# Optimization experiments

Measured on AMD Instinct MI355X. Metric: run time of the kernel, lower is better.

## Reference

```python
import jax, jax.numpy as jnp
import numpy as np

N_NODES = 50000
N_EDGES = 800000
N_GRAPHS = 1024
H = 128          # hidden_dim
L = 5            # n_conv_layers
NODE_IN = 4
EDGE_IN = 41
N_TARGETS = 3
EPS = 1e-5


def _ln(x, g, b):
    m = jnp.mean(x, axis=-1, keepdims=True)
    v = jnp.var(x, axis=-1, keepdims=True)
    return (x - m) / jnp.sqrt(v + EPS) * g + b


def setup_inputs() -> dict:
    key = jax.random.key(0)
    ks = jax.random.split(key, 24)
    w = lambda k, shp: (jax.random.normal(k, shp, dtype=jnp.float32) * 0.05)
    inp = {
        "atom_fea": jax.random.normal(ks[0], (N_NODES, NODE_IN), dtype=jnp.float32),
        "nbr_fea": jax.random.normal(ks[1], (N_EDGES, EDGE_IN), dtype=jnp.float32),
        "nbr_idx": jax.random.randint(ks[2], (N_EDGES, 2), 0, N_NODES, dtype=jnp.int32),
        "batch_mapping": jnp.sort(jax.random.randint(ks[3], (N_NODES,), 0, N_GRAPHS, dtype=jnp.int32)),
        # node embedding: Linear(4->H) + LayerNorm + SiLU
        "emb_w": w(ks[4], (NODE_IN, H)), "emb_b": jnp.zeros((H,), jnp.float32),
        "emb_ln_g": jnp.ones((H,), jnp.float32), "emb_ln_b": jnp.zeros((H,), jnp.float32),
        # edge embedding: Linear(41->H) + SiLU
        "edge_w": w(ks[5], (EDGE_IN, H)), "edge_b": jnp.zeros((H,), jnp.float32),
        # conv layers: Linear(2H->2H), SiLU, Linear(2H->H), SiLU; stacked over L
        "conv_w1": w(ks[6], (L, 2 * H, 2 * H)), "conv_b1": jnp.zeros((L, 2 * H), jnp.float32),
        "conv_w2": w(ks[7], (L, 2 * H, H)), "conv_b2": jnp.zeros((L, H), jnp.float32),
        "ln_g": jnp.ones((L, H), jnp.float32), "ln_b": jnp.zeros((L, H), jnp.float32),
        # output head
        "out_w1": w(ks[8], (H, H)), "out_b1": jnp.zeros((H,), jnp.float32),
        "out_w2": w(ks[9], (H, H // 2)), "out_b2": jnp.zeros((H // 2,), jnp.float32),
        "out_w3": w(ks[10], (H // 2, N_TARGETS)), "out_b3": jnp.zeros((N_TARGETS,), jnp.float32),
    }
    return inp


def reference(atom_fea, nbr_fea, nbr_idx, batch_mapping,
              emb_w, emb_b, emb_ln_g, emb_ln_b, edge_w, edge_b,
              conv_w1, conv_b1, conv_w2, conv_b2, ln_g, ln_b,
              out_w1, out_b1, out_w2, out_b2, out_w3, out_b3):
    silu = jax.nn.silu
    # embeddings (dropout is eval-mode identity)
    x = silu(_ln(atom_fea @ emb_w + emb_b, emb_ln_g, emb_ln_b))      # [N, H]
    e = silu(nbr_fea @ edge_w + edge_b)                               # [E, H]
    src, dst = nbr_idx[:, 0], nbr_idx[:, 1]
    n = x.shape[0]
    # per-node incoming edge counts (same every layer)
    cnt = jax.ops.segment_sum(jnp.ones_like(dst, dtype=x.dtype), dst, num_segments=n)
    cnt = jnp.clip(cnt, 1.0)[:, None]
    for i in range(L):
        m = jnp.concatenate([x[src], e], axis=1)                      # [E, 2H] gather
        m = silu(m @ conv_w1[i] + conv_b1[i])                         # [E, 2H]
        m = silu(m @ conv_w2[i] + conv_b2[i])                         # [E, H]
        aggr = jax.ops.segment_sum(m, dst, num_segments=n) / cnt      # scatter-mean
        x = _ln(x + aggr, ln_g[i], ln_b[i])                           # residual + LN
    # graph-level mean pooling
    gcnt = jax.ops.segment_sum(jnp.ones((n,), x.dtype), batch_mapping, num_segments=N_GRAPHS)
    gcnt = jnp.clip(gcnt, 1.0)[:, None]
    crystal = jax.ops.segment_sum(x, batch_mapping, num_segments=N_GRAPHS) / gcnt  # [G, H]
    h = silu(crystal @ out_w1 + out_b1)
    h = silu(h @ out_w2 + out_b2)
    return h @ out_w3 + out_b3                                        # [G, n_targets]
```

## Files before the change

kernel.cpp:

```cpp
#include <hip/hip_runtime.h>
#include <hip/hip_bf16.h>
#include <math.h>

#define N_NODES 50000
#define N_EDGES 800000
#define N_GRAPHS 1024
#define HD 128
#define NLAYERS 5
#define EDGE_IN 41
#define NT 3
#define LN_EPS 1e-5f

typedef unsigned int uint;
typedef unsigned short ushort;
typedef __attribute__((ext_vector_type(8))) short short8;
typedef __attribute__((ext_vector_type(4))) float f32x4;

__device__ __forceinline__ float silu_f(float v) {
    return v * __builtin_amdgcn_rcpf(1.0f + __expf(-v));
}

__device__ __forceinline__ ushort f2bf(float f) {
    uint u = __float_as_uint(f);
    u = u + 0x7FFFu + ((u >> 16) & 1u);
    return (ushort)(u >> 16);
}

__device__ __forceinline__ short8 ld16(const ushort* p) {
    union { int4 i; short8 s; } u;
    u.i = *(const int4*)p;
    return u.s;
}

__device__ __forceinline__ f32x4 mfma16(short8 a, short8 b, f32x4 c) {
    return __builtin_amdgcn_mfma_f32_16x16x32_bf16(a, b, c, 0, 0, 0);
}

__device__ __forceinline__ void wave_lds_fence() {
    __asm__ volatile("s_waitcnt lgkmcnt(0)" ::: "memory");
}

__device__ __forceinline__ void cp16(const ushort* g, ushort* l) {
    __builtin_amdgcn_global_load_lds(
        (const __attribute__((address_space(1))) unsigned int*)g,
        (__attribute__((address_space(3))) unsigned int*)l, 16, 0, 0);
}

__device__ __forceinline__ void stage4k(ushort* lds, const ushort* g, int w, int L) {
#pragma unroll
    for (int i = 0; i < 2; ++i) {
        int f = w * 1024 + i * 512;
        cp16(g + f + L * 8, lds + f);
    }
}

__global__ void k_zero(float* __restrict__ p, int n) {
    int i = blockIdx.x * 256 + threadIdx.x;
    if (i < n) p[i] = 0.0f;
}

__global__ void k_swz_w1(const float* __restrict__ w1, ushort* __restrict__ w1s) {
    int i = blockIdx.x * 256 + threadIdx.x;
    int l = i >> 16;
    int r = i & 65535;
    int j = r & 7, L = (r >> 3) & 63, s = (r >> 9) & 7, c = (r >> 12) & 15;
    int k = 32 * s + ((L >> 4) & 3) * 8 + j;
    int n = 16 * c + (L & 15);
    w1s[i] = f2bf(w1[(size_t)l * 65536 + k * 256 + n]);
}
__global__ void k_swz_w2(const float* __restrict__ w2, ushort* __restrict__ w2s) {
    int i = blockIdx.x * 256 + threadIdx.x;
    int l = i >> 15;
    int r = i & 32767;
    int j = r & 7, L = (r >> 3) & 63, t = (r >> 9) & 7, s2 = (r >> 12) & 7;
    int k = 32 * s2 + ((L >> 4) & 3) * 8 + j;
    int n = 16 * t + (L & 15);
    w2s[i] = f2bf(w2[(size_t)l * 32768 + k * 128 + n]);
}

__global__ __launch_bounds__(128) void k_node_embed(
    const float* __restrict__ atom, const float* __restrict__ w,
    const float* __restrict__ b, const float* __restrict__ g,
    const float* __restrict__ bet, float* __restrict__ x, ushort* __restrict__ x_bf)
{
    int node = blockIdx.x;
    int h = threadIdx.x;
    float4 a = *(const float4*)(atom + (size_t)node * 4);
    float acc = b[h] + a.x * w[h] + a.y * w[HD + h] + a.z * w[2 * HD + h] + a.w * w[3 * HD + h];
    __shared__ float s1[2], s2[2];
    float sum = acc, sq = acc * acc;
    for (int off = 32; off > 0; off >>= 1) { sum += __shfl_down(sum, off); sq += __shfl_down(sq, off); }
    int wid = h >> 6, lane = h & 63;
    if (lane == 0) { s1[wid] = sum; s2[wid] = sq; }
    __syncthreads();
    float m = (s1[0] + s1[1]) * (1.0f / 128.0f);
    float v = (s2[0] + s2[1]) * (1.0f / 128.0f) - m * m;
    float y = (acc - m) * rsqrtf(v + LN_EPS) * g[h] + bet[h];
    y = silu_f(y);
    x[(size_t)node * HD + h] = y;
    x_bf[(size_t)node * HD + h] = f2bf(y);
}

#define ETILE 32
__global__ __launch_bounds__(128) void k_edge_embed(
    const float* __restrict__ fea, const float* __restrict__ w,
    const float* __restrict__ b, ushort* __restrict__ e_bf)
{
    __shared__ float sf[ETILE][EDGE_IN + 1];
    int e0 = blockIdx.x * ETILE;
    int tid = threadIdx.x;
    for (int i = tid; i < ETILE * EDGE_IN; i += 128) {
        int m = i / EDGE_IN, k = i % EDGE_IN;
        sf[m][k] = fea[(size_t)(e0 + m) * EDGE_IN + k];
    }
    __syncthreads();
    float bb = b[tid];
    float acc[ETILE];
#pragma unroll
    for (int m = 0; m < ETILE; m++) acc[m] = bb;
    for (int k = 0; k < EDGE_IN; k++) {
        float wk = w[k * HD + tid];
#pragma unroll
        for (int m = 0; m < ETILE; m++) acc[m] += sf[m][k] * wk;
    }
#pragma unroll
    for (int m = 0; m < ETILE; m++)
        e_bf[(size_t)(e0 + m) * HD + tid] = f2bf(silu_f(acc[m]));
}

__global__ void k_count(const int* __restrict__ nbr_idx, float* __restrict__ cnt) {
    int i = blockIdx.x * 256 + threadIdx.x;
    if (i < N_EDGES) atomicAdd(&cnt[nbr_idx[2 * i + 1]], 1.0f);
}
__global__ void k_gcount(const int* __restrict__ bm, float* __restrict__ gcnt) {
    int i = blockIdx.x * 256 + threadIdx.x;
    if (i < N_NODES) atomicAdd(&gcnt[bm[i]], 1.0f);
}

#define M1CP 40
__global__ __launch_bounds__(256, 3) void k_conv_mfma(
    const ushort* __restrict__ x_bf, const ushort* __restrict__ e_bf,
    const int* __restrict__ nbr_idx,
    const ushort* __restrict__ w1s, const float* __restrict__ cb1,
    const ushort* __restrict__ w2s, const float* __restrict__ cb2,
    float* __restrict__ aggr)
{
    __shared__ __align__(16) ushort sW1[2][4096];
    __shared__ __align__(16) ushort sW2[2][4096];
    __shared__ __align__(16) ushort sM1[4][32 * M1CP];
    __shared__ int sDst[128];

    int tid = threadIdx.x;
    int w = tid >> 6;
    int L = tid & 63;
    int m = L & 15;
    int quad = L >> 4;
    int eb = blockIdx.x * 128;
    int ew = eb + w * 32;

    if (tid < 128) sDst[tid] = nbr_idx[2 * (eb + tid) + 1];

    short8 af[2][8];
#pragma unroll
    for (int t = 0; t < 2; ++t) {
        int src = nbr_idx[2 * (ew + t * 16 + m)];
        const ushort* xr = x_bf + (size_t)src * HD + quad * 8;
        const ushort* er = e_bf + (size_t)(ew + t * 16 + m) * HD + quad * 8;
#pragma unroll
        for (int s = 0; s < 4; ++s) af[t][s] = ld16(xr + 32 * s);
#pragma unroll
        for (int s = 0; s < 4; ++s) af[t][4 + s] = ld16(er + 32 * s);
    }

    f32x4 acc2[2][8];
#pragma unroll
    for (int t = 0; t < 2; ++t)
#pragma unroll
        for (int tt = 0; tt < 8; ++tt)
#pragma unroll
            for (int r = 0; r < 4; ++r) acc2[t][tt][r] = 0.0f;

    ushort* sm = sM1[w];

    stage4k(sW1[0], w1s, w, L);
    stage4k(sW2[0], w2s, w, L);

    for (int p = 0; p < 16; ++p) {
        __syncthreads();
        if (p < 15) stage4k(sW1[(p + 1) & 1], w1s + (p + 1) * 4096, w, L);
        if ((p & 1) && (p >> 1) < 7)
            stage4k(sW2[((p >> 1) + 1) & 1], w2s + ((p >> 1) + 1) * 4096, w, L);

        f32x4 p0, p1;
#pragma unroll
        for (int r = 0; r < 4; ++r) { p0[r] = 0.0f; p1[r] = 0.0f; }
        const ushort* wb = sW1[p & 1] + L * 8;
#pragma unroll
        for (int s = 0; s < 8; ++s) {
            short8 wv = ld16(wb + s * 512);
            p0 = mfma16(af[0][s], wv, p0);
            p1 = mfma16(af[1][s], wv, p1);
        }

        float bv = cb1[p * 16 + m];
        int hb = (p & 1) * 16;
#pragma unroll
        for (int r = 0; r < 4; ++r) {
            sm[(quad * 4 + r) * M1CP + hb + m]        = f2bf(silu_f(p0[r] + bv));
            sm[(16 + quad * 4 + r) * M1CP + hb + m]   = f2bf(silu_f(p1[r] + bv));
        }

        if (p & 1) {
            wave_lds_fence();
            short8 a20 = ld16(sm + m * M1CP + quad * 8);
            short8 a21 = ld16(sm + (16 + m) * M1CP + quad * 8);
            const ushort* w2p = sW2[(p >> 1) & 1] + L * 8;
#pragma unroll
            for (int tt = 0; tt < 8; ++tt) {
                short8 bf = ld16(w2p + tt * 512);
                acc2[0][tt] = mfma16(a20, bf, acc2[0][tt]);
                acc2[1][tt] = mfma16(a21, bf, acc2[1][tt]);
            }
            wave_lds_fence();
        }
    }

#pragma unroll
    for (int t = 0; t < 2; ++t) {
#pragma unroll
        for (int tt = 0; tt < 8; ++tt) {
            float bv = cb2[tt * 16 + m];
#pragma unroll
            for (int r = 0; r < 4; ++r) {
                int dst = sDst[w * 32 + t * 16 + quad * 4 + r];
                atomicAdd(aggr + (size_t)dst * HD + tt * 16 + m,
                          silu_f(acc2[t][tt][r] + bv));
            }
        }
    }
}

__global__ __launch_bounds__(128) void k_post(
    float* __restrict__ aggr, const float* __restrict__ cnt,
    const float* __restrict__ g, const float* __restrict__ bet,
    float* __restrict__ x, ushort* __restrict__ x_bf)
{
    int node = blockIdx.x;
    int h = threadIdx.x;
    float inv = __builtin_amdgcn_rcpf(fmaxf(cnt[node], 1.0f));
    float av = aggr[(size_t)node * HD + h];
    aggr[(size_t)node * HD + h] = 0.0f;
    float acc = x[(size_t)node * HD + h] + av * inv;
    __shared__ float s1[2], s2[2];
    float sum = acc, sq = acc * acc;
    for (int off = 32; off > 0; off >>= 1) { sum += __shfl_down(sum, off); sq += __shfl_down(sq, off); }
    int wid = h >> 6, lane = h & 63;
    if (lane == 0) { s1[wid] = sum; s2[wid] = sq; }
    __syncthreads();
    float m = (s1[0] + s1[1]) * (1.0f / 128.0f);
    float v = (s2[0] + s2[1]) * (1.0f / 128.0f) - m * m;
    float y = (acc - m) * rsqrtf(v + LN_EPS) * g[h] + bet[h];
    x[(size_t)node * HD + h] = y;
    x_bf[(size_t)node * HD + h] = f2bf(y);
}

__global__ __launch_bounds__(128) void k_gaggr(
    const float* __restrict__ x, const int* __restrict__ bm,
    float* __restrict__ crystal)
{
    int node = blockIdx.x;
    int h = threadIdx.x;
    atomicAdd(&crystal[(size_t)bm[node] * HD + h], x[(size_t)node * HD + h]);
}

__global__ __launch_bounds__(128) void k_readout(
    const float* __restrict__ crystal, const float* __restrict__ gcnt,
    const float* __restrict__ w1, const float* __restrict__ b1,
    const float* __restrict__ w2, const float* __restrict__ b2,
    const float* __restrict__ w3, const float* __restrict__ b3,
    float* __restrict__ out)
{
    int gph = blockIdx.x;
    int t = threadIdx.x;
    __shared__ float sc[HD], sh1[HD], sh2[64];
    float inv = __builtin_amdgcn_rcpf(fmaxf(gcnt[gph], 1.0f));
    sc[t] = crystal[(size_t)gph * HD + t] * inv;
    __syncthreads();
    float acc = b1[t];
    for (int k = 0; k < HD; k++) acc += sc[k] * w1[k * HD + t];
    sh1[t] = silu_f(acc);
    __syncthreads();
    if (t < 64) {
        float a2 = b2[t];
        for (int k = 0; k < HD; k++) a2 += sh1[k] * w2[k * 64 + t];
        sh2[t] = silu_f(a2);
    }
    __syncthreads();
    if (t < NT) {
        float a3 = b3[t];
        for (int k = 0; k < 64; k++) a3 += sh2[k] * w3[k * NT + t];
        out[(size_t)gph * NT + t] = a3;
    }
}

extern "C" void kernel_launch(void* const* d_in, const int* in_sizes, int n_in,
                              void* d_out, int out_size, void* d_ws, size_t ws_size,
                              hipStream_t stream)
{
    const float* atom_fea = (const float*)d_in[0];
    const float* nbr_fea  = (const float*)d_in[1];
    const int*   nbr_idx  = (const int*)d_in[2];
    const int*   bm       = (const int*)d_in[3];
    const float* emb_w    = (const float*)d_in[4];
    const float* emb_b    = (const float*)d_in[5];
    const float* emb_ln_g = (const float*)d_in[6];
    const float* emb_ln_b = (const float*)d_in[7];
    const float* edge_w   = (const float*)d_in[8];
    const float* edge_b   = (const float*)d_in[9];
    const float* conv_w1  = (const float*)d_in[10];
    const float* conv_b1  = (const float*)d_in[11];
    const float* conv_w2  = (const float*)d_in[12];
    const float* conv_b2  = (const float*)d_in[13];
    const float* ln_g     = (const float*)d_in[14];
    const float* ln_b     = (const float*)d_in[15];
    const float* out_w1   = (const float*)d_in[16];
    const float* out_b1   = (const float*)d_in[17];
    const float* out_w2   = (const float*)d_in[18];
    const float* out_b2   = (const float*)d_in[19];
    const float* out_w3   = (const float*)d_in[20];
    const float* out_b3   = (const float*)d_in[21];
    float* out = (float*)d_out;

    char* base = (char*)d_ws;
    size_t off = 0;
    auto alloc = [&](size_t bytes) -> char* {
        char* p = base + off;
        off = (off + bytes + 255) & ~(size_t)255;
        return p;
    };
    float*  xbuf    = (float*) alloc((size_t)N_NODES * HD * 4);
    float*  aggr    = (float*) alloc((size_t)N_NODES * HD * 4);
    float*  cnt     = (float*) alloc((size_t)N_NODES * 4);
    float*  crystal = (float*) alloc((size_t)N_GRAPHS * HD * 4);
    float*  gcnt    = (float*) alloc((size_t)N_GRAPHS * 4);
    ushort* x_bf    = (ushort*)alloc((size_t)N_NODES * HD * 2);
    ushort* e_bf    = (ushort*)alloc((size_t)N_EDGES * HD * 2);
    ushort* w1s     = (ushort*)alloc((size_t)NLAYERS * 65536 * 2);
    ushort* w2s     = (ushort*)alloc((size_t)NLAYERS * 32768 * 2);

    k_swz_w1<<<(NLAYERS * 65536) / 256, 256, 0, stream>>>(conv_w1, w1s);
    k_swz_w2<<<(NLAYERS * 32768) / 256, 256, 0, stream>>>(conv_w2, w2s);

    k_zero<<<(N_NODES * HD) / 256, 256, 0, stream>>>(aggr, N_NODES * HD);
    int zn = N_NODES + N_GRAPHS * HD + N_GRAPHS + 128;
    k_zero<<<(zn + 255) / 256, 256, 0, stream>>>(cnt, zn);

    k_node_embed<<<N_NODES, 128, 0, stream>>>(atom_fea, emb_w, emb_b, emb_ln_g, emb_ln_b, xbuf, x_bf);
    k_edge_embed<<<N_EDGES / ETILE, 128, 0, stream>>>(nbr_fea, edge_w, edge_b, e_bf);
    k_count<<<N_EDGES / 256, 256, 0, stream>>>(nbr_idx, cnt);
    k_gcount<<<(N_NODES + 255) / 256, 256, 0, stream>>>(bm, gcnt);

    for (int l = 0; l < NLAYERS; ++l) {
        k_conv_mfma<<<N_EDGES / 128, 256, 0, stream>>>(
            x_bf, e_bf, nbr_idx,
            w1s + (size_t)l * 65536, conv_b1 + (size_t)l * 256,
            w2s + (size_t)l * 32768, conv_b2 + (size_t)l * 128,
            aggr);
        k_post<<<N_NODES, 128, 0, stream>>>(aggr, cnt, ln_g + (size_t)l * HD, ln_b + (size_t)l * HD, xbuf, x_bf);
    }

    k_gaggr<<<N_NODES, 128, 0, stream>>>(xbuf, bm, crystal);
    k_readout<<<N_GRAPHS, 128, 0, stream>>>(crystal, gcnt, out_w1, out_b1, out_w2, out_b2, out_w3, out_b3, out);
}
```

Measured before the change: 2.746 ms.

## Sort edges by destination and pre-reduce messages in LDS before atomics

Builds a destination-sorted edge order (histogram, single-block scan, atomic scatter) and writes edge embeddings and src/dst arrays in that order. The conv kernel then stages its output tile in LDS and run-length-sums consecutive edges with the same destination before issuing global atomicAdds. The aim is fewer, more local atomics on aggr. In exchange it adds preprocessing kernels, including a serial single-block scan, and extra block-wide syncs in the epilogue.

```diff
diff --git a/kernel.cpp b/kernel.cpp
--- a/kernel.cpp
+++ b/kernel.cpp
@@ -57,6 +57,57 @@
 __global__ void k_zero(float* __restrict__ p, int n) {
     int i = blockIdx.x * 256 + threadIdx.x;
     if (i < n) p[i] = 0.0f;
+}
+
+__global__ void k_hist(const int* __restrict__ nbr_idx, int* __restrict__ cnt_i) {
+    int i = blockIdx.x * 256 + threadIdx.x;
+    if (i < N_EDGES) atomicAdd(&cnt_i[nbr_idx[2 * i + 1]], 1);
+}
+
+__global__ __launch_bounds__(256) void k_scan(
+    const int* __restrict__ cnt_i, int* __restrict__ cur, float* __restrict__ cntf)
+{
+    __shared__ int warpsum[4];
+    __shared__ int srun;
+    int tid = threadIdx.x;
+    int lane = tid & 63, wv = tid >> 6;
+    if (tid == 0) srun = 0;
+    __syncthreads();
+    for (int base = 0; base < N_NODES; base += 256) {
+        int i = base + tid;
+        int c = (i < N_NODES) ? cnt_i[i] : 0;
+        int s = c;
+        for (int off = 1; off < 64; off <<= 1) {
+            int t = __shfl_up(s, off);
+            if (lane >= off) s += t;
+        }
+        if (lane == 63) warpsum[wv] = s;
+        __syncthreads();
+        int woff = 0;
+        for (int k = 0; k < wv; ++k) woff += warpsum[k];
+        int run = srun;
+        if (i < N_NODES) {
+            cur[i]  = run + woff + s - c;
+            cntf[i] = (float)c;
+        }
+        __syncthreads();
+        if (tid == 255) srun = run + woff + s;
+    }
+}
+
+__global__ void k_scatter(const int* __restrict__ nbr_idx, int* __restrict__ cur,
+                          int* __restrict__ ssrc, int* __restrict__ sdst,
+                          int* __restrict__ posof)
+{
+    int e = blockIdx.x * 256 + threadIdx.x;
+    if (e < N_EDGES) {
+        int s = nbr_idx[2 * e];
+        int d = nbr_idx[2 * e + 1];
+        int p = atomicAdd(&cur[d], 1);
+        ssrc[p] = s;
+        sdst[p] = d;
+        posof[e] = p;
+    }
 }
 
 __global__ void k_swz_w1(const float* __restrict__ w1, ushort* __restrict__ w1s) {
@@ -104,7 +155,8 @@
 #define ETILE 32
 __global__ __launch_bounds__(128) void k_edge_embed(
     const float* __restrict__ fea, const float* __restrict__ w,
-    const float* __restrict__ b, ushort* __restrict__ e_bf)
+    const float* __restrict__ b, const int* __restrict__ posof,
+    ushort* __restrict__ e_bf)
 {
     __shared__ float sf[ETILE][EDGE_IN + 1];
     int e0 = blockIdx.x * ETILE;
@@ -124,14 +176,12 @@
         for (int m = 0; m < ETILE; m++) acc[m] += sf[m][k] * wk;
     }
 #pragma unroll
-    for (int m = 0; m < ETILE; m++)
-        e_bf[(size_t)(e0 + m) * HD + tid] = f2bf(silu_f(acc[m]));
-}
-
-__global__ void k_count(const int* __restrict__ nbr_idx, float* __restrict__ cnt) {
-    int i = blockIdx.x * 256 + threadIdx.x;
-    if (i < N_EDGES) atomicAdd(&cnt[nbr_idx[2 * i + 1]], 1.0f);
-}
+    for (int m = 0; m < ETILE; m++) {
+        int p = posof[e0 + m];
+        e_bf[(size_t)p * HD + tid] = f2bf(silu_f(acc[m]));
+    }
+}
+
 __global__ void k_gcount(const int* __restrict__ bm, float* __restrict__ gcnt) {
     int i = blockIdx.x * 256 + threadIdx.x;
     if (i < N_NODES) atomicAdd(&gcnt[bm[i]], 1.0f);
@@ -140,7 +190,7 @@
 #define M1CP 40
 __global__ __launch_bounds__(256, 3) void k_conv_mfma(
     const ushort* __restrict__ x_bf, const ushort* __restrict__ e_bf,
-    const int* __restrict__ nbr_idx,
+    const int* __restrict__ ssrc, const int* __restrict__ sdst,
     const ushort* __restrict__ w1s, const float* __restrict__ cb1,
     const ushort* __restrict__ w2s, const float* __restrict__ cb2,
     float* __restrict__ aggr)
@@ -158,12 +208,12 @@
     int eb = blockIdx.x * 128;
     int ew = eb + w * 32;
 
-    if (tid < 128) sDst[tid] = nbr_idx[2 * (eb + tid) + 1];
+    if (tid < 128) sDst[tid] = sdst[eb + tid];
 
     short8 af[2][8];
 #pragma unroll
     for (int t = 0; t < 2; ++t) {
-        int src = nbr_idx[2 * (ew + t * 16 + m)];
+        int src = ssrc[ew + t * 16 + m];
         const ushort* xr = x_bf + (size_t)src * HD + quad * 8;
         const ushort* er = e_bf + (size_t)(ew + t * 16 + m) * HD + quad * 8;
 #pragma unroll
@@ -225,18 +275,35 @@
         }
     }
 
-#pragma unroll
-    for (int t = 0; t < 2; ++t) {
-#pragma unroll
-        for (int tt = 0; tt < 8; ++tt) {
-            float bv = cb2[tt * 16 + m];
-#pragma unroll
-            for (int r = 0; r < 4; ++r) {
-                int dst = sDst[w * 32 + t * 16 + quad * 4 + r];
-                atomicAdd(aggr + (size_t)dst * HD + tt * 16 + m,
-                          silu_f(acc2[t][tt][r] + bv));
+    float* sRed = (float*)sW1;
+    int tcol = tid & 15;
+    int row0 = (tid >> 4) * 8;
+#pragma unroll
+    for (int tt = 0; tt < 8; ++tt) {
+        __syncthreads();
+        float bv = cb2[tt * 16 + m];
+#pragma unroll
+        for (int t = 0; t < 2; ++t)
+#pragma unroll
+            for (int r = 0; r < 4; ++r)
+                sRed[(w * 32 + t * 16 + quad * 4 + r) * 17 + m] =
+                    silu_f(acc2[t][tt][r] + bv);
+        __syncthreads();
+        float s = sRed[row0 * 17 + tcol];
+        int cd = sDst[row0];
+        for (int i = 1; i < 8; ++i) {
+            int rr = row0 + i;
+            int d2 = sDst[rr];
+            float v = sRed[rr * 17 + tcol];
+            if (d2 == cd) {
+                s += v;
+            } else {
+                atomicAdd(aggr + (size_t)cd * HD + tt * 16 + tcol, s);
+                cd = d2;
+                s = v;
             }
         }
+        atomicAdd(aggr + (size_t)cd * HD + tt * 16 + tcol, s);
     }
 }
 
@@ -347,6 +414,11 @@
     ushort* e_bf    = (ushort*)alloc((size_t)N_EDGES * HD * 2);
     ushort* w1s     = (ushort*)alloc((size_t)NLAYERS * 65536 * 2);
     ushort* w2s     = (ushort*)alloc((size_t)NLAYERS * 32768 * 2);
+    int*    cnt_i   = (int*)   alloc((size_t)N_NODES * 4);
+    int*    cur     = (int*)   alloc((size_t)N_NODES * 4);
+    int*    ssrc    = (int*)   alloc((size_t)N_EDGES * 4);
+    int*    sdst    = (int*)   alloc((size_t)N_EDGES * 4);
+    int*    posof   = (int*)   alloc((size_t)N_EDGES * 4);
 
     k_swz_w1<<<(NLAYERS * 65536) / 256, 256, 0, stream>>>(conv_w1, w1s);
     k_swz_w2<<<(NLAYERS * 32768) / 256, 256, 0, stream>>>(conv_w2, w2s);
@@ -354,15 +426,19 @@
     k_zero<<<(N_NODES * HD) / 256, 256, 0, stream>>>(aggr, N_NODES * HD);
     int zn = N_NODES + N_GRAPHS * HD + N_GRAPHS + 128;
     k_zero<<<(zn + 255) / 256, 256, 0, stream>>>(cnt, zn);
+    k_zero<<<(N_NODES + 255) / 256, 256, 0, stream>>>((float*)cnt_i, N_NODES);
+
+    k_hist<<<N_EDGES / 256, 256, 0, stream>>>(nbr_idx, cnt_i);
+    k_scan<<<1, 256, 0, stream>>>(cnt_i, cur, cnt);
+    k_scatter<<<N_EDGES / 256, 256, 0, stream>>>(nbr_idx, cur, ssrc, sdst, posof);
 
     k_node_embed<<<N_NODES, 128, 0, stream>>>(atom_fea, emb_w, emb_b, emb_ln_g, emb_ln_b, xbuf, x_bf);
-    k_edge_embed<<<N_EDGES / ETILE, 128, 0, stream>>>(nbr_fea, edge_w, edge_b, e_bf);
-    k_count<<<N_EDGES / 256, 256, 0, stream>>>(nbr_idx, cnt);
+    k_edge_embed<<<N_EDGES / ETILE, 128, 0, stream>>>(nbr_fea, edge_w, edge_b, posof, e_bf);
     k_gcount<<<(N_NODES + 255) / 256, 256, 0, stream>>>(bm, gcnt);
 
     for (int l = 0; l < NLAYERS; ++l) {
         k_conv_mfma<<<N_EDGES / 128, 256, 0, stream>>>(
-            x_bf, e_bf, nbr_idx,
+            x_bf, e_bf, ssrc, sdst,
             w1s + (size_t)l * 65536, conv_b1 + (size_t)l * 256,
             w2s + (size_t)l * 32768, conv_b2 + (size_t)l * 128,
             aggr);
```

Result: faster. 2.356 ms (-14.2%).
